# Kernel optimization log

Hardware: AMD Instinct MI355X
Metric: run time of the kernel (lower is better)

Reference implementation:

```python
import jax, jax.numpy as jnp
import numpy as np

K = 16          # num_bins
BOUND = 5.0     # tail_bound
MBW = 1e-3      # min_bin_width
MBH = 1e-3      # min_bin_height
MD = 1e-3       # min_derivative


def setup_inputs() -> dict:
    key = jax.random.key(0)
    ks = jax.random.split(key, 6)
    B, N, CD, H = 4096, 1024, 64, 256
    OUT = 3 * K + 1  # 2K widths/heights + (K+1) derivatives

    def lin_w(k, fan_in, shape):
        return (jax.random.normal(k, shape, jnp.float32) / np.sqrt(fan_in)).astype(jnp.float32)

    return {
        "cond": jax.random.normal(ks[0], (B, CD), jnp.float32),
        "y": jax.random.normal(ks[1], (B, N), jnp.float32) * 2.0,
        "W1": lin_w(ks[2], CD, (CD, H)), "b1": jnp.zeros((H,), jnp.float32),
        "W2": lin_w(ks[3], H, (H, H)),   "b2": jnp.zeros((H,), jnp.float32),
        "W3": lin_w(ks[4], H, (H, OUT)), "b3": jnp.zeros((OUT,), jnp.float32),
    }


def reference(cond, y, W1, b1, W2, b2, W3, b3):
    # --- conditioner MLP (concat mode, depth=2, dropout=0 / eval) ---
    h = jax.nn.relu(cond @ W1 + b1)
    h = jax.nn.relu(h @ W2 + b2)
    p = h @ W3 + b3                      # (B, 3K+1)
    un_w, un_h, un_d = p[..., :K], p[..., K:2 * K], p[..., 2 * K:]

    left, right, bottom, top = -BOUND, BOUND, -BOUND, BOUND
    widths = MBW + (right - left - K * MBW) * jax.nn.softmax(un_w, axis=-1)    # (B, K)
    heights = MBH + (top - bottom - K * MBH) * jax.nn.softmax(un_h, axis=-1)   # (B, K)
    cumw = jnp.pad(jnp.cumsum(widths, axis=-1), ((0, 0), (1, 0))) + left       # (B, K+1)
    cumh = jnp.pad(jnp.cumsum(heights, axis=-1), ((0, 0), (1, 0))) + bottom    # (B, K+1)
    deriv = MD + jax.nn.softplus(un_d)                                         # (B, K+1)

    xc = jnp.clip(y, left, right)                                              # (B, N)
    # bin search: O(K) broadcasted compare+sum, as in the original
    bin_idx = jnp.sum(xc[..., None] >= cumw[:, None, 1:], axis=-1)             # (B, N) int
    bin_idx = jnp.clip(bin_idx, 0, K - 1)

    gat = lambda a, i: jnp.take_along_axis(a, i, axis=-1)  # (B,K')[(B,N)] -> (B,N)
    x0 = gat(cumw, bin_idx)
    w = gat(widths, bin_idx)
    y0 = gat(cumh, bin_idx)
    hh = gat(heights, bin_idx)
    d0 = gat(deriv, bin_idx)
    d1 = gat(deriv, bin_idx + 1)

    delta = hh / w
    theta = (xc - x0) / w
    omt = 1.0 - theta
    num = hh * (delta * theta * theta + d0 * theta * omt)
    den = delta + (d0 + d1 - 2.0 * delta) * theta * omt
    out = y0 + num / den

    der_num = jnp.maximum(delta * delta * (d1 * theta * theta + 2.0 * delta * theta * omt + d0 * omt * omt), 1e-12)
    der_den = jnp.maximum(den * den, 1e-12)
    logdet = jnp.log(der_num) - jnp.log(der_den)

    outside = (y < left) | (y > right)
    out = jnp.where(outside, y, out)
    logdet = jnp.where(outside, jnp.zeros_like(logdet), logdet)
    return out, logdet
```

## Files before the change

### kernel.cpp

```cpp
#include <hip/hip_runtime.h>
#include <math.h>

namespace {
constexpr int KB    = 16;
constexpr int OUTP  = 3*KB + 1;
constexpr int CDIM  = 64;
constexpr int HDIM  = 256;
constexpr int NCOL  = 1024;
constexpr int NROW  = 4096;
constexpr float BOUNDF = 5.0f;
constexpr float MBW_ = 0.001f;
constexpr float MBH_ = 0.001f;
constexpr float MD_  = 0.001f;
constexpr int PSTR = 51;
constexpr int NR   = 8;
}

__global__ __launch_bounds__(256) void mlp_params_kernel(
    const float* __restrict__ cond,
    const float* __restrict__ W1, const float* __restrict__ b1,
    const float* __restrict__ W2, const float* __restrict__ b2,
    const float* __restrict__ W3, const float* __restrict__ b3,
    float* __restrict__ params)
{
    __shared__ float cond_s[NR][CDIM];
    __shared__ float ps[4][NR][HDIM];
    __shared__ float h_s[NR][HDIM];
    __shared__ float p_s[NR][OUTP];
    __shared__ float prm_s[NR][PSTR];

    const int tid  = threadIdx.x;
    const int lane = tid & 63;
    const int wid  = tid >> 6;
    const int row0 = blockIdx.x * NR;

    if (tid < NR*CDIM/4)
        *((float4*)&cond_s[0][0] + tid) = *((const float4*)(cond + (size_t)row0*CDIM) + tid);
    __syncthreads();

    {
        float acc[NR][4];
        #pragma unroll
        for (int r = 0; r < NR; ++r)
            #pragma unroll
            for (int c = 0; c < 4; ++c) acc[r][c] = 0.f;

        #pragma unroll
        for (int kg = 0; kg < 4; ++kg) {
            const int k0 = 16*wid + 4*kg;
            float4 wv[4];
            #pragma unroll
            for (int kk = 0; kk < 4; ++kk)
                wv[kk] = *(const float4*)(W1 + (size_t)(k0+kk)*HDIM + 4*lane);
            #pragma unroll
            for (int r = 0; r < NR; ++r) {
                const float4 cv4 = *(const float4*)&cond_s[r][k0];
                const float cv[4] = {cv4.x, cv4.y, cv4.z, cv4.w};
                const float wf[4][4] = {{wv[0].x,wv[0].y,wv[0].z,wv[0].w},
                                        {wv[1].x,wv[1].y,wv[1].z,wv[1].w},
                                        {wv[2].x,wv[2].y,wv[2].z,wv[2].w},
                                        {wv[3].x,wv[3].y,wv[3].z,wv[3].w}};
                #pragma unroll
                for (int kk = 0; kk < 4; ++kk)
                    #pragma unroll
                    for (int c = 0; c < 4; ++c)
                        acc[r][c] = fmaf(cv[kk], wf[kk][c], acc[r][c]);
            }
        }
        #pragma unroll
        for (int r = 0; r < NR; ++r)
            *(float4*)&ps[wid][r][4*lane] = make_float4(acc[r][0], acc[r][1], acc[r][2], acc[r][3]);
    }
    __syncthreads();
    {
        const float bb = b1[tid];
        #pragma unroll
        for (int r = 0; r < NR; ++r)
            h_s[r][tid] = fmaxf(ps[0][r][tid] + ps[1][r][tid] + ps[2][r][tid] + ps[3][r][tid] + bb, 0.f);
    }
    __syncthreads();

    {
        float acc[NR][4];
        #pragma unroll
        for (int r = 0; r < NR; ++r)
            #pragma unroll
            for (int c = 0; c < 4; ++c) acc[r][c] = 0.f;

        float4 wn[4];
        #pragma unroll
        for (int kk = 0; kk < 4; ++kk)
            wn[kk] = *(const float4*)(W2 + (size_t)(64*wid+kk)*HDIM + 4*lane);

        #pragma unroll 2
        for (int kg = 0; kg < 16; ++kg) {
            const int k0 = 64*wid + 4*kg;
            float4 wv[4];
            #pragma unroll
            for (int kk = 0; kk < 4; ++kk) wv[kk] = wn[kk];
            if (kg < 15) {
                #pragma unroll
                for (int kk = 0; kk < 4; ++kk)
                    wn[kk] = *(const float4*)(W2 + (size_t)(k0+4+kk)*HDIM + 4*lane);
            }
            #pragma unroll
            for (int r = 0; r < NR; ++r) {
                const float4 hv4 = *(const float4*)&h_s[r][k0];
                const float hv[4] = {hv4.x, hv4.y, hv4.z, hv4.w};
                const float wf[4][4] = {{wv[0].x,wv[0].y,wv[0].z,wv[0].w},
                                        {wv[1].x,wv[1].y,wv[1].z,wv[1].w},
                                        {wv[2].x,wv[2].y,wv[2].z,wv[2].w},
                                        {wv[3].x,wv[3].y,wv[3].z,wv[3].w}};
                #pragma unroll
                for (int kk = 0; kk < 4; ++kk)
                    #pragma unroll
                    for (int c = 0; c < 4; ++c)
                        acc[r][c] = fmaf(hv[kk], wf[kk][c], acc[r][c]);
            }
        }
        #pragma unroll
        for (int r = 0; r < NR; ++r)
            *(float4*)&ps[wid][r][4*lane] = make_float4(acc[r][0], acc[r][1], acc[r][2], acc[r][3]);
    }
    __syncthreads();
    {
        const float bb = b2[tid];
        #pragma unroll
        for (int r = 0; r < NR; ++r)
            h_s[r][tid] = fmaxf(ps[0][r][tid] + ps[1][r][tid] + ps[2][r][tid] + ps[3][r][tid] + bb, 0.f);
    }
    __syncthreads();

    {
        const int  o   = lane;
        const bool act = (o < OUTP);
        float acc[NR];
        #pragma unroll
        for (int r = 0; r < NR; ++r) acc[r] = 0.f;

        #pragma unroll 4
        for (int kg = 0; kg < 16; ++kg) {
            const int k0 = 64*wid + 4*kg;
            float wv[4];
            #pragma unroll
            for (int kk = 0; kk < 4; ++kk)
                wv[kk] = act ? W3[(size_t)(k0+kk)*OUTP + o] : 0.f;
            #pragma unroll
            for (int r = 0; r < NR; ++r) {
                const float4 hv = *(const float4*)&h_s[r][k0];
                acc[r] = fmaf(hv.x, wv[0], acc[r]);
                acc[r] = fmaf(hv.y, wv[1], acc[r]);
                acc[r] = fmaf(hv.z, wv[2], acc[r]);
                acc[r] = fmaf(hv.w, wv[3], acc[r]);
            }
        }
        if (act) {
            #pragma unroll
            for (int r = 0; r < NR; ++r) ps[wid][r][o] = acc[r];
        }
    }
    __syncthreads();
    for (int t = tid; t < NR*OUTP; t += 256) {
        const int r = t / OUTP;
        const int o = t - r*OUTP;
        p_s[r][o] = ps[0][r][o] + ps[1][r][o] + ps[2][r][o] + ps[3][r][o] + b3[o];
    }
    __syncthreads();

    if (tid < NR*3) {
        const int r   = tid / 3;
        const int seg = tid - 3*r;
        if (seg < 2) {
            const int   off   = (seg == 0) ? 0 : KB;
            const int   cbase = (seg == 0) ? 0 : 17;
            const float mb    = (seg == 0) ? MBW_ : MBH_;
            float m = -1e30f;
            #pragma unroll
            for (int i = 0; i < KB; ++i) m = fmaxf(m, p_s[r][off+i]);
            float e[KB];
            float s = 0.f;
            #pragma unroll
            for (int i = 0; i < KB; ++i) { e[i] = __expf(p_s[r][off+i] - m); s += e[i]; }
            const float span = (2.f*BOUNDF - (float)KB*mb) / s;
            float c = -BOUNDF;
            prm_s[r][cbase] = c;
            #pragma unroll
            for (int i = 0; i < KB; ++i) {
                c += mb + span*e[i];
                prm_s[r][cbase + 1 + i] = c;
            }
        } else {
            #pragma unroll
            for (int i = 0; i < KB+1; ++i) {
                const float x  = p_s[r][2*KB + i];
                const float sp = (x > 20.f) ? x : __logf(1.f + __expf(x));
                prm_s[r][34 + i] = MD_ + sp;
            }
        }
    }
    __syncthreads();

    for (int i = tid; i < NR*PSTR; i += 256)
        params[(size_t)row0*PSTR + i] = (&prm_s[0][0])[i];
}

__global__ __launch_bounds__(256) void spline_kernel(
    const float* __restrict__ y,
    const float* __restrict__ params,
    float* __restrict__ out,
    float* __restrict__ logdet)
{
    __shared__ float prm[PSTR];
    __shared__ float rec[KB][8];
    __shared__ float scan_s[KB];

    const int b   = blockIdx.x;
    const int tid = threadIdx.x;
    if (tid < PSTR) prm[tid] = params[(size_t)b*PSTR + tid];
    __syncthreads();
    if (tid < KB) {
        const int k = tid;
        rec[k][0] = prm[k];        rec[k][1] = prm[k+1];
        rec[k][2] = prm[17+k];     rec[k][3] = prm[17+k+1];
        rec[k][4] = prm[34+k];     rec[k][5] = prm[34+k+1];
        rec[k][6] = 0.f;           rec[k][7] = 0.f;
        scan_s[k] = prm[k+1];
    }
    __syncthreads();

    float cw[KB];
    #pragma unroll
    for (int q = 0; q < 4; ++q) {
        const float4 t4 = *(const float4*)&scan_s[4*q];
        cw[4*q+0] = t4.x; cw[4*q+1] = t4.y; cw[4*q+2] = t4.z; cw[4*q+3] = t4.w;
    }

    const size_t base = (size_t)b * NCOL + 4*tid;
    const float4 yv   = *(const float4*)(y + base);
    const float  yy[4] = {yv.x, yv.y, yv.z, yv.w};
    float ov[4], lv[4];

    #pragma unroll
    for (int i = 0; i < 4; ++i) {
        const float yi = yy[i];
        const bool outside = (yi < -BOUNDF) || (yi > BOUNDF);
        const float xc = fminf(fmaxf(yi, -BOUNDF), BOUNDF);
        int bin = 0;
        #pragma unroll
        for (int k = 0; k < KB; ++k) bin += (xc >= cw[k]) ? 1 : 0;
        bin = min(bin, KB-1);

        const float4 lo = *(const float4*)&rec[bin][0];
        const float2 hi = *(const float2*)&rec[bin][4];
        const float w  = lo.y - lo.x;
        const float hh = lo.w - lo.z;
        const float d0 = hi.x, d1 = hi.y;

        const float inv_w = __fdividef(1.f, w);
        const float delta = hh * inv_w;
        const float theta = (xc - lo.x) * inv_w;
        const float omt   = 1.f - theta;
        const float tt    = theta * theta;
        const float tomt  = theta * omt;
        const float num   = hh * (delta*tt + d0*tomt);
        const float den   = delta + (d0 + d1 - 2.f*delta)*tomt;
        const float o     = lo.z + __fdividef(num, den);
        const float der_num = fmaxf(delta*delta*(d1*tt + 2.f*delta*tomt + d0*omt*omt), 1e-12f);
        const float der_den = fmaxf(den*den, 1e-12f);
        const float ld      = __logf(__fdividef(der_num, der_den));

        ov[i] = outside ? yi : o;
        lv[i] = outside ? 0.f : ld;
    }

    *(float4*)(out + base)    = make_float4(ov[0], ov[1], ov[2], ov[3]);
    *(float4*)(logdet + base) = make_float4(lv[0], lv[1], lv[2], lv[3]);
}

extern "C" void kernel_launch(void* const* d_in, const int* in_sizes, int n_in,
                              void* d_out, int out_size, void* d_ws, size_t ws_size,
                              hipStream_t stream) {
    const float* cond = (const float*)d_in[0];
    const float* y    = (const float*)d_in[1];
    const float* W1   = (const float*)d_in[2];
    const float* b1   = (const float*)d_in[3];
    const float* W2   = (const float*)d_in[4];
    const float* b2   = (const float*)d_in[5];
    const float* W3   = (const float*)d_in[6];
    const float* b3   = (const float*)d_in[7];

    float* out    = (float*)d_out;
    float* logdet = out + (size_t)NROW * NCOL;
    float* params = (float*)d_ws;

    mlp_params_kernel<<<NROW/NR, 256, 0, stream>>>(cond, W1, b1, W2, b2, W3, b3, params);
    spline_kernel<<<NROW, 256, 0, stream>>>(y, params, out, logdet);
}
```

Before: 38.02 us.

## Split MLP K-reduction across 8 waves with two-stage shared-memory accumulation

The MLP parameter kernel now runs 512 threads per block instead of 256. Each of the eight waves handles half the K-slice it had before, and each layer's partial sums are merged in two steps: waves 0-3 write to shared memory, then waves 4-7 add their partials into the same slots. The goal is more latency hiding and a shorter serial FMA chain per thread on the small per-block GEMMs. The cost is extra __syncthreads barriers and read-modify-write traffic to shared memory, and the 4-blocks-per-CU launch bound may limit registers.

New measurement: 45.70 us. 1.2x slower.

```diff
diff --git a/kernel.cpp b/kernel.cpp
--- a/kernel.cpp
+++ b/kernel.cpp
@@ -14,9 +14,10 @@
 constexpr float MD_  = 0.001f;
 constexpr int PSTR = 51;
 constexpr int NR   = 8;
+constexpr int NT   = 512;
 }
 
-__global__ __launch_bounds__(256) void mlp_params_kernel(
+__global__ __launch_bounds__(NT, 4) void mlp_params_kernel(
     const float* __restrict__ cond,
     const float* __restrict__ W1, const float* __restrict__ b1,
     const float* __restrict__ W2, const float* __restrict__ b2,
@@ -32,6 +33,7 @@
     const int tid  = threadIdx.x;
     const int lane = tid & 63;
     const int wid  = tid >> 6;
+    const int slot = wid & 3;
     const int row0 = blockIdx.x * NR;
 
     if (tid < NR*CDIM/4)
@@ -46,8 +48,8 @@
             for (int c = 0; c < 4; ++c) acc[r][c] = 0.f;
 
         #pragma unroll
-        for (int kg = 0; kg < 4; ++kg) {
-            const int k0 = 16*wid + 4*kg;
+        for (int kg = 0; kg < 2; ++kg) {
+            const int k0 = 8*wid + 4*kg;
             float4 wv[4];
             #pragma unroll
             for (int kk = 0; kk < 4; ++kk)
@@ -67,38 +69,55 @@
                         acc[r][c] = fmaf(cv[kk], wf[kk][c], acc[r][c]);
             }
         }
+        if (wid < 4) {
+            #pragma unroll
+            for (int r = 0; r < NR; ++r)
+                *(float4*)&ps[slot][r][4*lane] = make_float4(acc[r][0], acc[r][1], acc[r][2], acc[r][3]);
+        }
+        __syncthreads();
+        if (wid >= 4) {
+            #pragma unroll
+            for (int r = 0; r < NR; ++r) {
+                float4 p = *(const float4*)&ps[slot][r][4*lane];
+                p.x += acc[r][0]; p.y += acc[r][1]; p.z += acc[r][2]; p.w += acc[r][3];
+                *(float4*)&ps[slot][r][4*lane] = p;
+            }
+        }
+        __syncthreads();
+    }
+    {
+        const int r  = tid >> 6;
+        const int c0 = 4*(tid & 63);
+        const float4 a = *(const float4*)&ps[0][r][c0];
+        const float4 b = *(const float4*)&ps[1][r][c0];
+        const float4 c = *(const float4*)&ps[2][r][c0];
+        const float4 d = *(const float4*)&ps[3][r][c0];
+        const float4 bb = *(const float4*)(b1 + c0);
+        *(float4*)&h_s[r][c0] = make_float4(
+            fmaxf(a.x+b.x+c.x+d.x+bb.x, 0.f), fmaxf(a.y+b.y+c.y+d.y+bb.y, 0.f),
+            fmaxf(a.z+b.z+c.z+d.z+bb.z, 0.f), fmaxf(a.w+b.w+c.w+d.w+bb.w, 0.f));
+    }
+    __syncthreads();
+
+    {
+        float acc[NR][4];
         #pragma unroll
         for (int r = 0; r < NR; ++r)
-            *(float4*)&ps[wid][r][4*lane] = make_float4(acc[r][0], acc[r][1], acc[r][2], acc[r][3]);
-    }
-    __syncthreads();
-    {
-        const float bb = b1[tid];
-        #pragma unroll
-        for (int r = 0; r < NR; ++r)
-            h_s[r][tid] = fmaxf(ps[0][r][tid] + ps[1][r][tid] + ps[2][r][tid] + ps[3][r][tid] + bb, 0.f);
-    }
-    __syncthreads();
-
-    {
-        float acc[NR][4];
-        #pragma unroll
-        for (int r = 0; r < NR; ++r)
             #pragma unroll
             for (int c = 0; c < 4; ++c) acc[r][c] = 0.f;
 
         float4 wn[4];
         #pragma unroll
         for (int kk = 0; kk < 4; ++kk)
-            wn[kk] = *(const float4*)(W2 + (size_t)(64*wid+kk)*HDIM + 4*lane);
-
-        #pragma unroll 2
-        for (int kg = 0; kg < 16; ++kg) {
-            const int k0 = 64*wid + 4*kg;
+            wn[kk] = *(const float4*)(W2 + (size_t)(32*wid+kk)*HDIM + 4*lane);
+
+        #pragma unroll
+        for (int kg = 0; kg < 8; ++kg) {
+            const int k0 = 32*wid + 4*kg;
             float4 wv[4];
             #pragma unroll
             for (int kk = 0; kk < 4; ++kk) wv[kk] = wn[kk];
-            if (kg < 15) {
+            if (kg < 7) {
                 #pragma unroll
                 for (int kk = 0; kk < 4; ++kk)
                     wn[kk] = *(const float4*)(W2 + (size_t)(k0+4+kk)*HDIM + 4*lane);
@@ -118,16 +137,35 @@
                         acc[r][c] = fmaf(hv[kk], wf[kk][c], acc[r][c]);
             }
         }
-        #pragma unroll
-        for (int r = 0; r < NR; ++r)
-            *(float4*)&ps[wid][r][4*lane] = make_float4(acc[r][0], acc[r][1], acc[r][2], acc[r][3]);
-    }
-    __syncthreads();
-    {
-        const float bb = b2[tid];
-        #pragma unroll
-        for (int r = 0; r < NR; ++r)
-            h_s[r][tid] = fmaxf(ps[0][r][tid] + ps[1][r][tid] + ps[2][r][tid] + ps[3][r][tid] + bb, 0.f);
+        if (wid < 4) {
+            #pragma unroll
+            for (int r = 0; r < NR; ++r)
+                *(float4*)&ps[slot][r][4*lane] = make_float4(acc[r][0], acc[r][1], acc[r][2], acc[r][3]);
+        }
+        __syncthreads();
+        if (wid >= 4) {
+            #pragma unroll
+            for (int r = 0; r < NR; ++r) {
+                float4 p = *(const float4*)&ps[slot][r][4*lane];
+                p.x += acc[r][0]; p.y += acc[r][1]; p.z += acc[r][2]; p.w += acc[r][3];
+                *(float4*)&ps[slot][r][4*lane] = p;
+            }
+        }
+        __syncthreads();
+    }
+    {
+        const int r  = tid >> 6;
+        const int c0 = 4*(tid & 63);
+        const float4 a = *(const float4*)&ps[0][r][c0];
+        const float4 b = *(const float4*)&ps[1][r][c0];
+        const float4 c = *(const float4*)&ps[2][r][c0];
+        const float4 d = *(const float4*)&ps[3][r][c0];
+        const float4 bb = *(const float4*)(b2 + c0);
+        const float4 hn = make_float4(
+            fmaxf(a.x+b.x+c.x+d.x+bb.x, 0.f), fmaxf(a.y+b.y+c.y+d.y+bb.y, 0.f),
+            fmaxf(a.z+b.z+c.z+d.z+bb.z, 0.f), fmaxf(a.w+b.w+c.w+d.w+bb.w, 0.f));
+        __syncthreads();
+        *(float4*)&h_s[r][c0] = hn;
     }
     __syncthreads();
 
@@ -139,8 +177,8 @@
         for (int r = 0; r < NR; ++r) acc[r] = 0.f;
 
         #pragma unroll 4
-        for (int kg = 0; kg < 16; ++kg) {
-            const int k0 = 64*wid + 4*kg;
+        for (int kg = 0; kg < 8; ++kg) {
+            const int k0 = 32*wid + 4*kg;
             float wv[4];
             #pragma unroll
             for (int kk = 0; kk < 4; ++kk)
@@ -155,12 +193,19 @@
             }
         }
         if (act) {
-            #pragma unroll
-            for (int r = 0; r < NR; ++r) ps[wid][r][o] = acc[r];
-        }
-    }
-    __syncthreads();
-    for (int t = tid; t < NR*OUTP; t += 256) {
+            if (wid < 4) {
+                #pragma unroll
+                for (int r = 0; r < NR; ++r) ps[slot][r][o] = acc[r];
+            }
+        }
+        __syncthreads();
+        if (act && wid >= 4) {
+            #pragma unroll
+            for (int r = 0; r < NR; ++r) ps[slot][r][o] += acc[r];
+        }
+        __syncthreads();
+    }
+    for (int t = tid; t < NR*OUTP; t += NT) {
         const int r = t / OUTP;
         const int o = t - r*OUTP;
         p_s[r][o] = ps[0][r][o] + ps[1][r][o] + ps[2][r][o] + ps[3][r][o] + b3[o];
@@ -200,7 +245,7 @@
     }
     __syncthreads();
 
-    for (int i = tid; i < NR*PSTR; i += 256)
+    for (int i = tid; i < NR*PSTR; i += NT)
         params[(size_t)row0*PSTR + i] = (&prm_s[0][0])[i];
 }
 
@@ -293,6 +338,6 @@
     float* logdet = out + (size_t)NROW * NCOL;
     float* params = (float*)d_ws;
 
-    mlp_params_kernel<<<NROW/NR, 256, 0, stream>>>(cond, W1, b1, W2, b2, W3, b3, params);
+    mlp_params_kernel<<<NROW/NR, NT, 0, stream>>>(cond, W1, b1, W2, b2, W3, b3, params);
     spline_kernel<<<NROW, 256, 0, stream>>>(y, params, out, logdet);
 }
```

## Run conditioner MLP on bf16 MFMA with hi/lo split for fp32 accuracy

Applied to the files above, without the earlier changes.

Replaces the scalar-FMA MLP kernel with one that uses 16x16x32 bf16 MFMA instructions, splitting every operand into high and low bf16 parts and summing three products to approximate fp32 accuracy. A new prep kernel runs on every call and transposes and splits the weights into bf16 hi/lo buffers in workspace. Hidden activations are kept in shared memory as packed hi/lo pairs, and each block now handles 16 rows instead of 8. This targets the FMA-bound MLP stage, at the cost of an extra kernel launch plus weight-conversion traffic and a small precision loss from dropping the lo*lo term.

New measurement: 42.41 us. +11.5%, slower.

```diff
diff --git a/kernel.cpp b/kernel.cpp
--- a/kernel.cpp
+++ b/kernel.cpp
@@ -12,162 +12,193 @@
 constexpr float MBW_ = 0.001f;
 constexpr float MBH_ = 0.001f;
 constexpr float MD_  = 0.001f;
-constexpr int PSTR = 51;
-constexpr int NR   = 8;
-}
-
-__global__ __launch_bounds__(256) void mlp_params_kernel(
+constexpr int PSTR  = 51;
+constexpr int MROWS = 16;
+constexpr int HSTR  = 260;
+constexpr int N3    = 64;
+}
+
+typedef __attribute__((ext_vector_type(8))) short bf16x8;
+typedef __attribute__((ext_vector_type(4))) float f32x4;
+
+__device__ __forceinline__ unsigned short f32_to_bf16_rne(float v) {
+    unsigned u = __float_as_uint(v);
+    return (unsigned short)((u + 0x7FFFu + ((u >> 16) & 1u)) >> 16);
+}
+__device__ __forceinline__ float bf16_to_f32(unsigned short h) {
+    return __uint_as_float(((unsigned)h) << 16);
+}
+__device__ __forceinline__ void split_bf16(float v, unsigned short& hi, unsigned short& lo) {
+    hi = f32_to_bf16_rne(v);
+    lo = f32_to_bf16_rne(v - bf16_to_f32(hi));
+}
+__device__ __forceinline__ unsigned pack_split(float v) {
+    unsigned short h, l; split_bf16(v, h, l);
+    return (unsigned)h | ((unsigned)l << 16);
+}
+
+__global__ __launch_bounds__(256) void prep_weights(
+    const float* __restrict__ W1, const float* __restrict__ W2,
+    const float* __restrict__ W3,
+    unsigned short* __restrict__ w1hi, unsigned short* __restrict__ w1lo,
+    unsigned short* __restrict__ w2hi, unsigned short* __restrict__ w2lo,
+    unsigned short* __restrict__ w3hi, unsigned short* __restrict__ w3lo)
+{
+    const int t = blockIdx.x * 256 + threadIdx.x;
+    {
+        const int col = t >> 8, k = t & 255;
+        unsigned short h, l; split_bf16(W2[(size_t)k*HDIM + col], h, l);
+        w2hi[t] = h; w2lo[t] = l;
+    }
+    if (t < 256*64) {
+        const int col = t >> 6, k = t & 63;
+        unsigned short h, l; split_bf16(W1[(size_t)k*HDIM + col], h, l);
+        w1hi[t] = h; w1lo[t] = l;
+    }
+    if (t < N3*256) {
+        const int col = t >> 8, k = t & 255;
+        const float v = (col < OUTP) ? W3[(size_t)k*OUTP + col] : 0.f;
+        unsigned short h, l; split_bf16(v, h, l);
+        w3hi[t] = h; w3lo[t] = l;
+    }
+}
+
+__global__ __launch_bounds__(256) void mlp_mfma_kernel(
     const float* __restrict__ cond,
-    const float* __restrict__ W1, const float* __restrict__ b1,
-    const float* __restrict__ W2, const float* __restrict__ b2,
-    const float* __restrict__ W3, const float* __restrict__ b3,
+    const float* __restrict__ b1, const float* __restrict__ b2,
+    const float* __restrict__ b3,
+    const unsigned short* __restrict__ w1hi, const unsigned short* __restrict__ w1lo,
+    const unsigned short* __restrict__ w2hi, const unsigned short* __restrict__ w2lo,
+    const unsigned short* __restrict__ w3hi, const unsigned short* __restrict__ w3lo,
     float* __restrict__ params)
 {
-    __shared__ float cond_s[NR][CDIM];
-    __shared__ float ps[4][NR][HDIM];
-    __shared__ float h_s[NR][HDIM];
-    __shared__ float p_s[NR][OUTP];
-    __shared__ float prm_s[NR][PSTR];
+    __shared__ unsigned h1c[MROWS][HSTR];
+    __shared__ unsigned h2c[MROWS][HSTR];
+    __shared__ float    p_s[MROWS][OUTP];
+    __shared__ float    prm_s[MROWS][PSTR];
 
     const int tid  = threadIdx.x;
     const int lane = tid & 63;
     const int wid  = tid >> 6;
-    const int row0 = blockIdx.x * NR;
-
-    if (tid < NR*CDIM/4)
-        *((float4*)&cond_s[0][0] + tid) = *((const float4*)(cond + (size_t)row0*CDIM) + tid);
-    __syncthreads();
+    const int mrow = lane & 15;
+    const int kg   = lane >> 4;
+    const int row0 = blockIdx.x * MROWS;
 
     {
-        float acc[NR][4];
-        #pragma unroll
-        for (int r = 0; r < NR; ++r)
-            #pragma unroll
-            for (int c = 0; c < 4; ++c) acc[r][c] = 0.f;
-
-        #pragma unroll
-        for (int kg = 0; kg < 4; ++kg) {
-            const int k0 = 16*wid + 4*kg;
-            float4 wv[4];
-            #pragma unroll
-            for (int kk = 0; kk < 4; ++kk)
-                wv[kk] = *(const float4*)(W1 + (size_t)(k0+kk)*HDIM + 4*lane);
-            #pragma unroll
-            for (int r = 0; r < NR; ++r) {
-                const float4 cv4 = *(const float4*)&cond_s[r][k0];
-                const float cv[4] = {cv4.x, cv4.y, cv4.z, cv4.w};
-                const float wf[4][4] = {{wv[0].x,wv[0].y,wv[0].z,wv[0].w},
-                                        {wv[1].x,wv[1].y,wv[1].z,wv[1].w},
-                                        {wv[2].x,wv[2].y,wv[2].z,wv[2].w},
-                                        {wv[3].x,wv[3].y,wv[3].z,wv[3].w}};
-                #pragma unroll
-                for (int kk = 0; kk < 4; ++kk)
-                    #pragma unroll
-                    for (int c = 0; c < 4; ++c)
-                        acc[r][c] = fmaf(cv[kk], wf[kk][c], acc[r][c]);
-            }
-        }
-        #pragma unroll
-        for (int r = 0; r < NR; ++r)
-            *(float4*)&ps[wid][r][4*lane] = make_float4(acc[r][0], acc[r][1], acc[r][2], acc[r][3]);
-    }
-    __syncthreads();
+        f32x4 acc[4];
+        #pragma unroll
+        for (int t = 0; t < 4; ++t) acc[t] = (f32x4)0.f;
+
+        #pragma unroll
+        for (int c = 0; c < CDIM/32; ++c) {
+            const float* ap = cond + (size_t)(row0 + mrow)*CDIM + c*32 + kg*8;
+            const float4 a0 = *(const float4*)ap;
+            const float4 a1 = *(const float4*)(ap + 4);
+            const float av[8] = {a0.x,a0.y,a0.z,a0.w,a1.x,a1.y,a1.z,a1.w};
+            bf16x8 Ahi, Alo;
+            #pragma unroll
+            for (int j = 0; j < 8; ++j) {
+                unsigned short h, l; split_bf16(av[j], h, l);
+                Ahi[j] = (short)h; Alo[j] = (short)l;
+            }
+            #pragma unroll
+            for (int t = 0; t < 4; ++t) {
+                const int colb = wid*64 + t*16 + mrow;
+                const size_t off = (size_t)colb*CDIM + c*32 + kg*8;
+                const bf16x8 Bhi = *(const bf16x8*)(w1hi + off);
+                const bf16x8 Blo = *(const bf16x8*)(w1lo + off);
+                acc[t] = __builtin_amdgcn_mfma_f32_16x16x32_bf16(Alo, Bhi, acc[t], 0, 0, 0);
+                acc[t] = __builtin_amdgcn_mfma_f32_16x16x32_bf16(Ahi, Blo, acc[t], 0, 0, 0);
+                acc[t] = __builtin_amdgcn_mfma_f32_16x16x32_bf16(Ahi, Bhi, acc[t], 0, 0, 0);
+            }
+        }
+        #pragma unroll
+        for (int t = 0; t < 4; ++t) {
+            const int col = wid*64 + t*16 + mrow;
+            const float bb = b1[col];
+            #pragma unroll
+            for (int r = 0; r < 4; ++r) {
+                const int row = kg*4 + r;
+                const float v = fmaxf(acc[t][r] + bb, 0.f);
+                h1c[row][col] = pack_split(v);
+            }
+        }
+    }
+    __syncthreads();
+
     {
-        const float bb = b1[tid];
-        #pragma unroll
-        for (int r = 0; r < NR; ++r)
-            h_s[r][tid] = fmaxf(ps[0][r][tid] + ps[1][r][tid] + ps[2][r][tid] + ps[3][r][tid] + bb, 0.f);
+        f32x4 acc[4];
+        #pragma unroll
+        for (int t = 0; t < 4; ++t) acc[t] = (f32x4)0.f;
+
+        #pragma unroll 2
+        for (int c = 0; c < HDIM/32; ++c) {
+            const uint4 u0 = *(const uint4*)&h1c[mrow][c*32 + kg*8];
+            const uint4 u1 = *(const uint4*)&h1c[mrow][c*32 + kg*8 + 4];
+            const unsigned uu[8] = {u0.x,u0.y,u0.z,u0.w,u1.x,u1.y,u1.z,u1.w};
+            bf16x8 Ahi, Alo;
+            #pragma unroll
+            for (int j = 0; j < 8; ++j) {
+                Ahi[j] = (short)(uu[j] & 0xFFFFu);
+                Alo[j] = (short)(uu[j] >> 16);
+            }
+            #pragma unroll
+            for (int t = 0; t < 4; ++t) {
+                const int colb = wid*64 + t*16 + mrow;
+                const size_t off = (size_t)colb*HDIM + c*32 + kg*8;
+                const bf16x8 Bhi = *(const bf16x8*)(w2hi + off);
+                const bf16x8 Blo = *(const bf16x8*)(w2lo + off);
+                acc[t] = __builtin_amdgcn_mfma_f32_16x16x32_bf16(Alo, Bhi, acc[t], 0, 0, 0);
+                acc[t] = __builtin_amdgcn_mfma_f32_16x16x32_bf16(Ahi, Blo, acc[t], 0, 0, 0);
+                acc[t] = __builtin_amdgcn_mfma_f32_16x16x32_bf16(Ahi, Bhi, acc[t], 0, 0, 0);
+            }
+        }
+        #pragma unroll
+        for (int t = 0; t < 4; ++t) {
+            const int col = wid*64 + t*16 + mrow;
+            const float bb = b2[col];
+            #pragma unroll
+            for (int r = 0; r < 4; ++r) {
+                const int row = kg*4 + r;
+                const float v = fmaxf(acc[t][r] + bb, 0.f);
+                h2c[row][col] = pack_split(v);
+            }
+        }
     }
     __syncthreads();
 
     {
-        float acc[NR][4];
-        #pragma unroll
-        for (int r = 0; r < NR; ++r)
-            #pragma unroll
-            for (int c = 0; c < 4; ++c) acc[r][c] = 0.f;
-
-        float4 wn[4];
-        #pragma unroll
-        for (int kk = 0; kk < 4; ++kk)
-            wn[kk] = *(const float4*)(W2 + (size_t)(64*wid+kk)*HDIM + 4*lane);
-
+        f32x4 acc = (f32x4)0.f;
         #pragma unroll 2
-        for (int kg = 0; kg < 16; ++kg) {
-            const int k0 = 64*wid + 4*kg;
-            float4 wv[4];
-            #pragma unroll
-            for (int kk = 0; kk < 4; ++kk) wv[kk] = wn[kk];
-            if (kg < 15) {
-                #pragma unroll
-                for (int kk = 0; kk < 4; ++kk)
-                    wn[kk] = *(const float4*)(W2 + (size_t)(k0+4+kk)*HDIM + 4*lane);
-            }
-            #pragma unroll
-            for (int r = 0; r < NR; ++r) {
-                const float4 hv4 = *(const float4*)&h_s[r][k0];
-                const float hv[4] = {hv4.x, hv4.y, hv4.z, hv4.w};
-                const float wf[4][4] = {{wv[0].x,wv[0].y,wv[0].z,wv[0].w},
-                                        {wv[1].x,wv[1].y,wv[1].z,wv[1].w},
-                                        {wv[2].x,wv[2].y,wv[2].z,wv[2].w},
-                                        {wv[3].x,wv[3].y,wv[3].z,wv[3].w}};
-                #pragma unroll
-                for (int kk = 0; kk < 4; ++kk)
-                    #pragma unroll
-                    for (int c = 0; c < 4; ++c)
-                        acc[r][c] = fmaf(hv[kk], wf[kk][c], acc[r][c]);
-            }
-        }
-        #pragma unroll
-        for (int r = 0; r < NR; ++r)
-            *(float4*)&ps[wid][r][4*lane] = make_float4(acc[r][0], acc[r][1], acc[r][2], acc[r][3]);
-    }
-    __syncthreads();
-    {
-        const float bb = b2[tid];
-        #pragma unroll
-        for (int r = 0; r < NR; ++r)
-            h_s[r][tid] = fmaxf(ps[0][r][tid] + ps[1][r][tid] + ps[2][r][tid] + ps[3][r][tid] + bb, 0.f);
-    }
-    __syncthreads();
-
-    {
-        const int  o   = lane;
-        const bool act = (o < OUTP);
-        float acc[NR];
-        #pragma unroll
-        for (int r = 0; r < NR; ++r) acc[r] = 0.f;
-
-        #pragma unroll 4
-        for (int kg = 0; kg < 16; ++kg) {
-            const int k0 = 64*wid + 4*kg;
-            float wv[4];
-            #pragma unroll
-            for (int kk = 0; kk < 4; ++kk)
-                wv[kk] = act ? W3[(size_t)(k0+kk)*OUTP + o] : 0.f;
-            #pragma unroll
-            for (int r = 0; r < NR; ++r) {
-                const float4 hv = *(const float4*)&h_s[r][k0];
-                acc[r] = fmaf(hv.x, wv[0], acc[r]);
-                acc[r] = fmaf(hv.y, wv[1], acc[r]);
-                acc[r] = fmaf(hv.z, wv[2], acc[r]);
-                acc[r] = fmaf(hv.w, wv[3], acc[r]);
-            }
-        }
-        if (act) {
-            #pragma unroll
-            for (int r = 0; r < NR; ++r) ps[wid][r][o] = acc[r];
-        }
-    }
-    __syncthreads();
-    for (int t = tid; t < NR*OUTP; t += 256) {
-        const int r = t / OUTP;
-        const int o = t - r*OUTP;
-        p_s[r][o] = ps[0][r][o] + ps[1][r][o] + ps[2][r][o] + ps[3][r][o] + b3[o];
-    }
-    __syncthreads();
-
-    if (tid < NR*3) {
+        for (int c = 0; c < HDIM/32; ++c) {
+            const uint4 u0 = *(const uint4*)&h2c[mrow][c*32 + kg*8];
+            const uint4 u1 = *(const uint4*)&h2c[mrow][c*32 + kg*8 + 4];
+            const unsigned uu[8] = {u0.x,u0.y,u0.z,u0.w,u1.x,u1.y,u1.z,u1.w};
+            bf16x8 Ahi, Alo;
+            #pragma unroll
+            for (int j = 0; j < 8; ++j) {
+                Ahi[j] = (short)(uu[j] & 0xFFFFu);
+                Alo[j] = (short)(uu[j] >> 16);
+            }
+            const int colb = wid*16 + mrow;
+            const size_t off = (size_t)colb*HDIM + c*32 + kg*8;
+            const bf16x8 Bhi = *(const bf16x8*)(w3hi + off);
+            const bf16x8 Blo = *(const bf16x8*)(w3lo + off);
+            acc = __builtin_amdgcn_mfma_f32_16x16x32_bf16(Alo, Bhi, acc, 0, 0, 0);
+            acc = __builtin_amdgcn_mfma_f32_16x16x32_bf16(Ahi, Blo, acc, 0, 0, 0);
+            acc = __builtin_amdgcn_mfma_f32_16x16x32_bf16(Ahi, Bhi, acc, 0, 0, 0);
+        }
+        const int col = wid*16 + mrow;
+        if (col < OUTP) {
+            const float bb = b3[col];
+            #pragma unroll
+            for (int r = 0; r < 4; ++r)
+                p_s[kg*4 + r][col] = acc[r] + bb;
+        }
+    }
+    __syncthreads();
+
+    if (tid < MROWS*3) {
         const int r   = tid / 3;
         const int seg = tid - 3*r;
         if (seg < 2) {
@@ -200,7 +231,7 @@
     }
     __syncthreads();
 
-    for (int i = tid; i < NR*PSTR; i += 256)
+    for (int i = tid; i < MROWS*PSTR; i += 256)
         params[(size_t)row0*PSTR + i] = (&prm_s[0][0])[i];
 }
 
@@ -291,8 +322,18 @@
 
     float* out    = (float*)d_out;
     float* logdet = out + (size_t)NROW * NCOL;
+
     float* params = (float*)d_ws;
-
-    mlp_params_kernel<<<NROW/NR, 256, 0, stream>>>(cond, W1, b1, W2, b2, W3, b3, params);
+    unsigned short* w1hi = (unsigned short*)((char*)d_ws + (1 << 20));
+    unsigned short* w1lo = w1hi + 64*HDIM;
+    unsigned short* w2hi = w1lo + 64*HDIM;
+    unsigned short* w2lo = w2hi + HDIM*HDIM;
+    unsigned short* w3hi = w2lo + HDIM*HDIM;
+    unsigned short* w3lo = w3hi + N3*HDIM;
+
+    prep_weights<<<256, 256, 0, stream>>>(W1, W2, W3, w1hi, w1lo, w2hi, w2lo, w3hi, w3lo);
+    mlp_mfma_kernel<<<NROW/MROWS, 256, 0, stream>>>(cond, b1, b2, b3,
+                                                    w1hi, w1lo, w2hi, w2lo, w3hi, w3lo,
+                                                    params);
     spline_kernel<<<NROW, 256, 0, stream>>>(y, params, out, logdet);
 }
```
